# Optimization experiments

Hardware: AMD Instinct MI355X
Metric: run time of the kernel (lower is better)

## Reference

```python
import jax, jax.numpy as jnp
import numpy as np

EPS = 1e-08


def setup_inputs() -> dict:
    key = jax.random.key(0)
    kx, ky = jax.random.split(key)
    x = jax.random.normal(kx, (8192, 512), dtype=jnp.float32)
    y = jax.random.normal(ky, (8192, 512), dtype=jnp.float32)
    return {"x": x, "y": y}


def reference(x, y):
    # Faithful to torch.nn.CosineSimilarity(dim=2, eps=EPS) applied to the
    # broadcast pair (x[i], y[j]):
    #   cos[i, j] = <x_i, y_j> / (max(||x_i||, eps) * max(||y_j||, eps))
    # Algebraically equivalent efficient form: normalize rows once, then GEMM.
    xn = x / jnp.maximum(jnp.linalg.norm(x, axis=1, keepdims=True), EPS)  # [Nx, L]
    yn = y / jnp.maximum(jnp.linalg.norm(y, axis=1, keepdims=True), EPS)  # [Ny, L]
    return jnp.einsum('il,jl->ij', xn, yn)  # [Nx, Ny]
```

## Files before the change

kernel.cpp:

```cpp
#include <hip/hip_runtime.h>


typedef __attribute__((ext_vector_type(8))) short bf16x8;
typedef __attribute__((ext_vector_type(4))) float f32x4;
typedef __attribute__((ext_vector_type(8))) unsigned short ushort8;

#define M_DIM 8192
#define N_DIM 8192
#define K_DIM 512

static __device__ __forceinline__ unsigned short f32_to_bf16(float f) {
  unsigned int u = __float_as_uint(f);
  u = (u + 0x7FFFu + ((u >> 16) & 1u)) >> 16;
  return (unsigned short)u;
}

__global__ __launch_bounds__(256) void normalize_rows(
    const float* __restrict__ x, const float* __restrict__ y,
    unsigned short* __restrict__ out) {
  const int wid = threadIdx.x >> 6;
  const int lane = threadIdx.x & 63;
  const int row = (blockIdx.x << 2) + wid;
  const float* src = row < M_DIM ? x + (size_t)row * K_DIM
                                 : y + (size_t)(row - M_DIM) * K_DIM;
  const float4* r = (const float4*)src;
  float4 v0 = r[lane * 2];
  float4 v1 = r[lane * 2 + 1];
  float ss = v0.x * v0.x + v0.y * v0.y + v0.z * v0.z + v0.w * v0.w +
             v1.x * v1.x + v1.y * v1.y + v1.z * v1.z + v1.w * v1.w;
#pragma unroll
  for (int off = 32; off; off >>= 1) ss += __shfl_xor(ss, off, 64);
  const float s = 1.0f / fmaxf(sqrtf(ss), 1e-8f);
  const float f[8] = {v0.x, v0.y, v0.z, v0.w, v1.x, v1.y, v1.z, v1.w};
  union { ushort8 v; unsigned short u[8]; } o;
#pragma unroll
  for (int i = 0; i < 8; ++i) o.u[i] = f32_to_bf16(f[i] * s);
  *(ushort8*)(out + (size_t)row * K_DIM + lane * 8) = o.v;
}

static __device__ __forceinline__ void gl16(const unsigned short* g, char* l) {
  __builtin_amdgcn_global_load_lds(
      (const __attribute__((address_space(1))) unsigned int*)g,
      (__attribute__((address_space(3))) unsigned int*)l, 16, 0, 0);
}

#define BAR() __builtin_amdgcn_s_barrier()
#define SBAR() __builtin_amdgcn_sched_barrier(0)
#define LGKM0() do { asm volatile("s_waitcnt lgkmcnt(0)" ::: "memory"); \
                     __builtin_amdgcn_sched_barrier(0); } while (0)
#define VMCNT(n) do { asm volatile("s_waitcnt vmcnt(" #n ")" ::: "memory"); \
                      __builtin_amdgcn_sched_barrier(0); } while (0)

__global__ __launch_bounds__(256, 2) void cosgemm(
    const unsigned short* __restrict__ A,
    const unsigned short* __restrict__ B,
    float* __restrict__ C) {
  extern __shared__ char smem[];

  const int tid = threadIdx.x;
  const int lane = tid & 63;
  const int wid = tid >> 6;
  const int wm = wid >> 1;
  const int wn = wid & 1;
  const int lr16 = lane & 15;
  const int hq = lane >> 4;
  const int sw = hq ^ (lr16 & 3);

  const int bid = blockIdx.x;
  const int idx = bid >> 3;
  const int by = ((bid & 7) << 2) + (idx & 3);
  const int bx = idx >> 2;
  const int row0 = by << 8;
  const int col0 = bx << 7;

  const int srl = lane >> 2;
  const int ssl = (lane & 3) ^ (srl & 3);
  const unsigned short* pA =
      A + (size_t)(row0 + (wid << 6) + srl) * K_DIM + ssl * 8;
  const unsigned short* pB =
      B + (size_t)(col0 + (wid << 5) + srl) * K_DIM + ssl * 8;

  auto stageA2 = [&](int par, int cpair, int T) {
    char* l = smem + par * 24576 + (wid << 12) + (cpair << 11);
    const unsigned short* g = pA + T * 32 + (size_t)(cpair << 5) * K_DIM;
    gl16(g, l);
    gl16(g + (size_t)16 * K_DIM, l + 1024);
  };
  auto stageB1 = [&](int par, int c, int T) {
    char* l = smem + par * 24576 + 16384 + (wid << 11) + (c << 10);
    gl16(pB + T * 32 + (size_t)(c << 4) * K_DIM, l);
  };

  bf16x8 af[4], bf[4];
  f32x4 acc[8][4] = {};

  auto ldA = [&](int par, int fmBase) {
#pragma unroll
    for (int j = 0; j < 4; ++j) {
      const int row = (wm << 7) + (fmBase + j) * 16 + lr16;
      af[j] = *(const bf16x8*)(smem + par * 24576 + row * 64 + (sw << 4));
    }
  };
  auto ldB = [&](int par, int fnBase) {
#pragma unroll
    for (int j = 0; j < 2; ++j) {
      const int row = (wn << 6) + (fnBase + j) * 16 + lr16;
      bf[fnBase + j] =
          *(const bf16x8*)(smem + par * 24576 + 16384 + row * 64 + (sw << 4));
    }
  };
  auto mm = [&](int fmBase, int fnBase) {
    __builtin_amdgcn_s_setprio(1);
#pragma unroll
    for (int m = 0; m < 4; ++m)
#pragma unroll
      for (int n = 0; n < 2; ++n)
        acc[fmBase + m][fnBase + n] = __builtin_amdgcn_mfma_f32_16x16x32_bf16(
            af[m], bf[fnBase + n], acc[fmBase + m][fnBase + n], 0, 0, 0);
    __builtin_amdgcn_s_setprio(0);
  };

  stageA2(0, 0, 0); stageA2(0, 1, 0);
  stageB1(0, 0, 0); stageB1(0, 1, 0);
  stageB1(1, 0, 1); stageB1(1, 1, 1);
  VMCNT(2);
  BAR(); SBAR();

#pragma unroll 1
  for (int j = 0; j < 8; ++j) {
    const bool st = (j < 7);
    const int u = 2 * j + 1, t2 = 2 * j + 2, t3 = 2 * j + 3;
    ldA(0, 0); ldB(0, 0); stageA2(1, 0, u);
    BAR(); LGKM0(); mm(0, 0); BAR();
    ldB(0, 2); stageA2(1, 1, u);
    BAR(); LGKM0(); mm(0, 2); BAR();
    ldA(0, 4); if (st) stageB1(0, 0, t2);
    BAR(); LGKM0(); mm(4, 0); BAR();
    if (st) stageB1(0, 1, t2);
    BAR(); LGKM0(); mm(4, 2);
    if (st) { VMCNT(2); } else { VMCNT(0); }
    BAR(); SBAR();
    ldA(1, 0); ldB(1, 0); if (st) stageA2(0, 0, t2);
    BAR(); LGKM0(); mm(0, 0); BAR();
    ldB(1, 2); if (st) stageA2(0, 1, t2);
    BAR(); LGKM0(); mm(0, 2); BAR();
    ldA(1, 4); if (st) stageB1(1, 0, t3);
    BAR(); LGKM0(); mm(4, 0); BAR();
    if (st) stageB1(1, 1, t3);
    BAR(); LGKM0(); mm(4, 2);
    if (st) { VMCNT(2); }
    BAR(); SBAR();
  }

  float* S = (float*)(smem + wid * 4352);
  const int crow0 = row0 + (wm << 7);
  const int ccol0 = col0 + (wn << 6);
#pragma unroll
  for (int fm = 0; fm < 8; ++fm) {
#pragma unroll
    for (int fn = 0; fn < 4; ++fn)
#pragma unroll
      for (int q = 0; q < 4; ++q)
        S[(hq * 4 + q) * 68 + fn * 16 + lr16] = acc[fm][fn][q];
#pragma unroll
    for (int r = 0; r < 4; ++r) {
      f32x4 v = *(const f32x4*)&S[(r * 4 + hq) * 68 + lr16 * 4];
      __builtin_nontemporal_store(
          v, (f32x4*)&C[(size_t)(crow0 + fm * 16 + r * 4 + hq) * N_DIM +
                        ccol0 + lr16 * 4]);
    }
  }
}

extern "C" void kernel_launch(void* const* d_in, const int* in_sizes, int n_in,
                              void* d_out, int out_size, void* d_ws, size_t ws_size,
                              hipStream_t stream) {
  const float* x = (const float*)d_in[0];
  const float* y = (const float*)d_in[1];
  float* out = (float*)d_out;
  unsigned short* xn = (unsigned short*)d_ws;
  unsigned short* yn = xn + (size_t)M_DIM * K_DIM;

  (void)hipFuncSetAttribute((const void*)cosgemm,
                            hipFuncAttributeMaxDynamicSharedMemorySize, 65536);

  normalize_rows<<<(M_DIM + N_DIM) / 4, 256, 0, stream>>>(x, y, xn);
  cosgemm<<<(M_DIM / 256) * (N_DIM / 128), 256, 49152, stream>>>(xn, yn, out);
}
```

Before: 109.5 us.

## Transpose GEMM block tile to 128x256 with 4x1 warp layout and wide-row epilogue

Changes the block tile from 256x128 to 128x256 and rearranges the warps from a 2x2 grid to four warps stacked along M, each computing 32 rows by the full 256 columns. The A/B staging roles and the block-index swizzle are swapped to match. The epilogue now stages 8-row slabs through LDS so each row write covers a contiguous 1 KB stretch, aimed at the large fp32 output write, and it uses plain stores instead of nontemporal ones. The cost is more LDS fragment reads per warp per k-step (B fragments are no longer shared across a warp pair) and more accumulator registers per warp.

```diff
diff --git a/kernel.cpp b/kernel.cpp
--- a/kernel.cpp
+++ b/kernel.cpp
@@ -60,69 +60,67 @@
   const int tid = threadIdx.x;
   const int lane = tid & 63;
   const int wid = tid >> 6;
-  const int wm = wid >> 1;
-  const int wn = wid & 1;
   const int lr16 = lane & 15;
   const int hq = lane >> 4;
   const int sw = hq ^ (lr16 & 3);
 
   const int bid = blockIdx.x;
   const int idx = bid >> 3;
-  const int by = ((bid & 7) << 2) + (idx & 3);
-  const int bx = idx >> 2;
-  const int row0 = by << 8;
-  const int col0 = bx << 7;
+  const int by = ((bid & 7) << 3) + (idx & 7);
+  const int bx = idx >> 3;
+  const int row0 = by << 7;
+  const int col0 = bx << 8;
 
   const int srl = lane >> 2;
   const int ssl = (lane & 3) ^ (srl & 3);
   const unsigned short* pA =
-      A + (size_t)(row0 + (wid << 6) + srl) * K_DIM + ssl * 8;
+      A + (size_t)(row0 + (wid << 5) + srl) * K_DIM + ssl * 8;
   const unsigned short* pB =
-      B + (size_t)(col0 + (wid << 5) + srl) * K_DIM + ssl * 8;
+      B + (size_t)(col0 + (wid << 6) + srl) * K_DIM + ssl * 8;
 
-  auto stageA2 = [&](int par, int cpair, int T) {
-    char* l = smem + par * 24576 + (wid << 12) + (cpair << 11);
-    const unsigned short* g = pA + T * 32 + (size_t)(cpair << 5) * K_DIM;
+  auto stageA1 = [&](int par, int c, int T) {
+    char* l = smem + par * 24576 + (wid << 11) + (c << 10);
+    gl16(pA + T * 32 + (size_t)(c << 4) * K_DIM, l);
+  };
+  auto stageB2 = [&](int par, int cp, int T) {
+    char* l = smem + par * 24576 + 8192 + (wid << 12) + (cp << 11);
+    const unsigned short* g = pB + T * 32 + (size_t)(cp << 5) * K_DIM;
     gl16(g, l);
     gl16(g + (size_t)16 * K_DIM, l + 1024);
   };
-  auto stageB1 = [&](int par, int c, int T) {
-    char* l = smem + par * 24576 + 16384 + (wid << 11) + (c << 10);
-    gl16(pB + T * 32 + (size_t)(c << 4) * K_DIM, l);
+
+  bf16x8 af[2], bf[4];
+  f32x4 acc[2][16] = {};
+
+  auto ldA = [&](int par) {
+#pragma unroll
+    for (int m = 0; m < 2; ++m) {
+      const int row = (wid << 5) + m * 16 + lr16;
+      af[m] = *(const bf16x8*)(smem + par * 24576 + row * 64 + (sw << 4));
+    }
   };
-
-  bf16x8 af[4], bf[4];
-  f32x4 acc[8][4] = {};
-
-  auto ldA = [&](int par, int fmBase) {
+  auto ldB = [&](int par, int g) {
 #pragma unroll
     for (int j = 0; j < 4; ++j) {
-      const int row = (wm << 7) + (fmBase + j) * 16 + lr16;
-      af[j] = *(const bf16x8*)(smem + par * 24576 + row * 64 + (sw << 4));
+      const int row = (g * 4 + j) * 16 + lr16;
+      bf[j] = *(const bf16x8*)(smem + par * 24576 + 8192 + row * 64 +
+                               (sw << 4));
     }
   };
-  auto ldB = [&](int par, int fnBase) {
-#pragma unroll
-    for (int j = 0; j < 2; ++j) {
-      const int row = (wn << 6) + (fnBase + j) * 16 + lr16;
-      bf[fnBase + j] =
-          *(const bf16x8*)(smem + par * 24576 + 16384 + row * 64 + (sw << 4));
-    }
-  };
-  auto mm = [&](int fmBase, int fnBase) {
+  auto mm = [&](int g) {
     __builtin_amdgcn_s_setprio(1);
 #pragma unroll
-    for (int m = 0; m < 4; ++m)
+    for (int m = 0; m < 2; ++m)
 #pragma unroll
-      for (int n = 0; n < 2; ++n)
-        acc[fmBase + m][fnBase + n] = __builtin_amdgcn_mfma_f32_16x16x32_bf16(
-            af[m], bf[fnBase + n], acc[fmBase + m][fnBase + n], 0, 0, 0);
+      for (int j = 0; j < 4; ++j)
+        acc[m][g * 4 + j] = __builtin_amdgcn_mfma_f32_16x16x32_bf16(
+            af[m], bf[j], acc[m][g * 4 + j], 0, 0, 0);
     __builtin_amdgcn_s_setprio(0);
   };
 
-  stageA2(0, 0, 0); stageA2(0, 1, 0);
-  stageB1(0, 0, 0); stageB1(0, 1, 0);
-  stageB1(1, 0, 1); stageB1(1, 1, 1);
+  stageB2(0, 0, 0); stageB2(0, 1, 0);
+  stageA1(0, 0, 0); stageA1(0, 1, 0);
+  stageA1(1, 0, 1); stageA1(1, 1, 1);
   VMCNT(2);
   BAR(); SBAR();
 
@@ -130,46 +128,49 @@
   for (int j = 0; j < 8; ++j) {
     const bool st = (j < 7);
     const int u = 2 * j + 1, t2 = 2 * j + 2, t3 = 2 * j + 3;
-    ldA(0, 0); ldB(0, 0); stageA2(1, 0, u);
-    BAR(); LGKM0(); mm(0, 0); BAR();
-    ldB(0, 2); stageA2(1, 1, u);
-    BAR(); LGKM0(); mm(0, 2); BAR();
-    ldA(0, 4); if (st) stageB1(0, 0, t2);
-    BAR(); LGKM0(); mm(4, 0); BAR();
-    if (st) stageB1(0, 1, t2);
-    BAR(); LGKM0(); mm(4, 2);
+    ldA(0); ldB(0, 0); stageB2(1, 0, u);
+    BAR(); LGKM0(); mm(0); BAR();
+    ldB(0, 1); stageB2(1, 1, u);
+    BAR(); LGKM0(); mm(1); BAR();
+    ldB(0, 2); if (st) stageA1(0, 0, t2);
+    BAR(); LGKM0(); mm(2); BAR();
+    ldB(0, 3); if (st) stageA1(0, 1, t2);
+    BAR(); LGKM0(); mm(3);
     if (st) { VMCNT(2); } else { VMCNT(0); }
     BAR(); SBAR();
-    ldA(1, 0); ldB(1, 0); if (st) stageA2(0, 0, t2);
-    BAR(); LGKM0(); mm(0, 0); BAR();
-    ldB(1, 2); if (st) stageA2(0, 1, t2);
-    BAR(); LGKM0(); mm(0, 2); BAR();
-    ldA(1, 4); if (st) stageB1(1, 0, t3);
-    BAR(); LGKM0(); mm(4, 0); BAR();
-    if (st) stageB1(1, 1, t3);
-    BAR(); LGKM0(); mm(4, 2);
+    ldA(1); ldB(1, 0); if (st) stageB2(0, 0, t2);
+    BAR(); LGKM0(); mm(0); BAR();
+    ldB(1, 1); if (st) stageB2(0, 1, t2);
+    BAR(); LGKM0(); mm(1); BAR();
+    ldB(1, 2); if (st) stageA1(1, 0, t3);
+    BAR(); LGKM0(); mm(2); BAR();
+    ldB(1, 3); if (st) stageA1(1, 1, t3);
+    BAR(); LGKM0(); mm(3);
     if (st) { VMCNT(2); }
     BAR(); SBAR();
   }
 
-  float* S = (float*)(smem + wid * 4352);
-  const int crow0 = row0 + (wm << 7);
-  const int ccol0 = col0 + (wn << 6);
+  float* S = (float*)(smem + wid * 8256);
+  const int crow0 = row0 + (wid << 5);
+  const size_t cbase = (size_t)col0 + lane * 4;
 #pragma unroll
-  for (int fm = 0; fm < 8; ++fm) {
+  for (int fm = 0; fm < 2; ++fm)
 #pragma unroll
-    for (int fn = 0; fn < 4; ++fn)
+    for (int h = 0; h < 2; ++h) {
+      if ((hq >> 1) == h) {
 #pragma unroll
-      for (int q = 0; q < 4; ++q)
-        S[(hq * 4 + q) * 68 + fn * 16 + lr16] = acc[fm][fn][q];
+        for (int fn = 0; fn < 16; ++fn)
 #pragma unroll
-    for (int r = 0; r < 4; ++r) {
-      f32x4 v = *(const f32x4*)&S[(r * 4 + hq) * 68 + lr16 * 4];
-      __builtin_nontemporal_store(
-          v, (f32x4*)&C[(size_t)(crow0 + fm * 16 + r * 4 + hq) * N_DIM +
-                        ccol0 + lr16 * 4]);
+          for (int q = 0; q < 4; ++q)
+            S[((hq & 1) * 4 + q) * 258 + fn * 16 + lr16] = acc[fm][fn][q];
+      }
+      LGKM0();
+#pragma unroll
+      for (int r = 0; r < 8; ++r) {
+        f32x4 v = *(const f32x4*)&S[r * 258 + lane * 4];
+        *(f32x4*)&C[(size_t)(crow0 + fm * 16 + h * 8 + r) * N_DIM + cbase] = v;
+      }
     }
-  }
 }
 
 extern "C" void kernel_launch(void* const* d_in, const int* in_sizes, int n_in,
@@ -185,5 +186,5 @@
                             hipFuncAttributeMaxDynamicSharedMemorySize, 65536);
 
   normalize_rows<<<(M_DIM + N_DIM) / 4, 256, 0, stream>>>(x, y, xn);
-  cosgemm<<<(M_DIM / 256) * (N_DIM / 128), 256, 49152, stream>>>(xn, yn, out);
+  cosgemm<<<(M_DIM / 128) * (N_DIM / 256), 256, 49152, stream>>>(xn, yn, out);
 }
```

Result: slower. 113.5 us (+3.6%).

## Shrink GEMM tile to 128x128 with triple-buffered LDS pipeline and higher occupancy

Applied to the files above, without the earlier changes.

The block tile drops from 256x128 to 128x128, halving the accumulators per wave so that three blocks can fit per CU (launch bounds raised to 3). The double-buffered ping-pong loop becomes a triple-buffered ring with prefetch distance two, and the block-index swizzle is adjusted for the doubled grid. Smaller tiles and more blocks aim to improve latency hiding and load balance across CUs, at the cost of lower arithmetic intensity per tile and more redundant global and L2 traffic.

```diff
diff --git a/kernel.cpp b/kernel.cpp
--- a/kernel.cpp
+++ b/kernel.cpp
@@ -51,7 +51,7 @@
 #define VMCNT(n) do { asm volatile("s_waitcnt vmcnt(" #n ")" ::: "memory"); \
                       __builtin_amdgcn_sched_barrier(0); } while (0)
 
-__global__ __launch_bounds__(256, 2) void cosgemm(
+__global__ __launch_bounds__(256, 3) void cosgemm(
     const unsigned short* __restrict__ A,
     const unsigned short* __restrict__ B,
     float* __restrict__ C) {
@@ -68,95 +68,80 @@
 
   const int bid = blockIdx.x;
   const int idx = bid >> 3;
-  const int by = ((bid & 7) << 2) + (idx & 3);
-  const int bx = idx >> 2;
-  const int row0 = by << 8;
+  const int by = ((bid & 7) << 3) + (idx & 7);
+  const int bx = idx >> 3;
+  const int row0 = by << 7;
   const int col0 = bx << 7;
 
   const int srl = lane >> 2;
   const int ssl = (lane & 3) ^ (srl & 3);
   const unsigned short* pA =
-      A + (size_t)(row0 + (wid << 6) + srl) * K_DIM + ssl * 8;
+      A + (size_t)(row0 + (wid << 4) + srl) * K_DIM + ssl * 8;
   const unsigned short* pB =
-      B + (size_t)(col0 + (wid << 5) + srl) * K_DIM + ssl * 8;
+      B + (size_t)(col0 + (wid << 4) + srl) * K_DIM + ssl * 8;
 
-  auto stageA2 = [&](int par, int cpair, int T) {
-    char* l = smem + par * 24576 + (wid << 12) + (cpair << 11);
-    const unsigned short* g = pA + T * 32 + (size_t)(cpair << 5) * K_DIM;
-    gl16(g, l);
-    gl16(g + (size_t)16 * K_DIM, l + 1024);
+  auto stageA = [&](int buf, int h, int T) {
+    char* l = smem + buf * 16384 + (h << 12) + (wid << 10);
+    gl16(pA + T * 32 + (size_t)(h << 6) * K_DIM, l);
   };
-  auto stageB1 = [&](int par, int c, int T) {
-    char* l = smem + par * 24576 + 16384 + (wid << 11) + (c << 10);
-    gl16(pB + T * 32 + (size_t)(c << 4) * K_DIM, l);
+  auto stageB = [&](int buf, int h, int T) {
+    char* l = smem + buf * 16384 + 8192 + (h << 12) + (wid << 10);
+    gl16(pB + T * 32 + (size_t)(h << 6) * K_DIM, l);
   };
 
   bf16x8 af[4], bf[4];
-  f32x4 acc[8][4] = {};
+  f32x4 acc[4][4] = {};
 
-  auto ldA = [&](int par, int fmBase) {
+  auto ldA = [&](int buf) {
 #pragma unroll
-    for (int j = 0; j < 4; ++j) {
-      const int row = (wm << 7) + (fmBase + j) * 16 + lr16;
-      af[j] = *(const bf16x8*)(smem + par * 24576 + row * 64 + (sw << 4));
+    for (int m = 0; m < 4; ++m) {
+      const int row = (wm << 6) + m * 16 + lr16;
+      af[m] = *(const bf16x8*)(smem + buf * 16384 + row * 64 + (sw << 4));
     }
   };
-  auto ldB = [&](int par, int fnBase) {
+  auto ldB = [&](int buf, int g) {
 #pragma unroll
     for (int j = 0; j < 2; ++j) {
-      const int row = (wn << 6) + (fnBase + j) * 16 + lr16;
-      bf[fnBase + j] =
-          *(const bf16x8*)(smem + par * 24576 + 16384 + row * 64 + (sw << 4));
+      const int row = (wn << 6) + (g * 2 + j) * 16 + lr16;
+      bf[g * 2 + j] = *(const bf16x8*)(smem + buf * 16384 + 8192 + row * 64 +
+                                       (sw << 4));
     }
   };
-  auto mm = [&](int fmBase, int fnBase) {
+  auto mm = [&](int g) {
     __builtin_amdgcn_s_setprio(1);
 #pragma unroll
     for (int m = 0; m < 4; ++m)
 #pragma unroll
-      for (int n = 0; n < 2; ++n)
-        acc[fmBase + m][fnBase + n] = __builtin_amdgcn_mfma_f32_16x16x32_bf16(
-            af[m], bf[fnBase + n], acc[fmBase + m][fnBase + n], 0, 0, 0);
+      for (int j = 0; j < 2; ++j)
+        acc[m][g * 2 + j] = __builtin_amdgcn_mfma_f32_16x16x32_bf16(
+            af[m], bf[g * 2 + j], acc[m][g * 2 + j], 0, 0, 0);
     __builtin_amdgcn_s_setprio(0);
   };
 
-  stageA2(0, 0, 0); stageA2(0, 1, 0);
-  stageB1(0, 0, 0); stageB1(0, 1, 0);
-  stageB1(1, 0, 1); stageB1(1, 1, 1);
-  VMCNT(2);
+  stageA(0, 0, 0); stageA(0, 1, 0); stageB(0, 0, 0); stageB(0, 1, 0);
+  stageA(1, 0, 1); stageA(1, 1, 1); stageB(1, 0, 1); stageB(1, 1, 1);
+  VMCNT(4);
   BAR(); SBAR();
 
 #pragma unroll 1
-  for (int j = 0; j < 8; ++j) {
-    const bool st = (j < 7);
-    const int u = 2 * j + 1, t2 = 2 * j + 2, t3 = 2 * j + 3;
-    ldA(0, 0); ldB(0, 0); stageA2(1, 0, u);
-    BAR(); LGKM0(); mm(0, 0); BAR();
-    ldB(0, 2); stageA2(1, 1, u);
-    BAR(); LGKM0(); mm(0, 2); BAR();
-    ldA(0, 4); if (st) stageB1(0, 0, t2);
-    BAR(); LGKM0(); mm(4, 0); BAR();
-    if (st) stageB1(0, 1, t2);
-    BAR(); LGKM0(); mm(4, 2);
-    if (st) { VMCNT(2); } else { VMCNT(0); }
-    BAR(); SBAR();
-    ldA(1, 0); ldB(1, 0); if (st) stageA2(0, 0, t2);
-    BAR(); LGKM0(); mm(0, 0); BAR();
-    ldB(1, 2); if (st) stageA2(0, 1, t2);
-    BAR(); LGKM0(); mm(0, 2); BAR();
-    ldA(1, 4); if (st) stageB1(1, 0, t3);
-    BAR(); LGKM0(); mm(4, 0); BAR();
-    if (st) stageB1(1, 1, t3);
-    BAR(); LGKM0(); mm(4, 2);
-    if (st) { VMCNT(2); }
+  for (int t = 0; t < 16; ++t) {
+    const int cb = t % 3, nb = (t + 2) % 3;
+    const bool st = (t < 14);
+    ldA(cb); ldB(cb, 0);
+    if (st) { stageA(nb, 0, t + 2); stageA(nb, 1, t + 2); }
+    BAR(); LGKM0(); mm(0); BAR();
+    ldB(cb, 1);
+    if (st) { stageB(nb, 0, t + 2); stageB(nb, 1, t + 2); }
+    BAR(); LGKM0(); mm(1);
+    if (st) { VMCNT(4); } else { VMCNT(0); }
     BAR(); SBAR();
   }
 
   float* S = (float*)(smem + wid * 4352);
-  const int crow0 = row0 + (wm << 7);
+  const int crow0 = row0 + (wm << 6);
   const int ccol0 = col0 + (wn << 6);
 #pragma unroll
-  for (int fm = 0; fm < 8; ++fm) {
+  for (int fm = 0; fm < 4; ++fm) {
 #pragma unroll
     for (int fn = 0; fn < 4; ++fn)
 #pragma unroll
@@ -182,8 +167,8 @@
   unsigned short* yn = xn + (size_t)M_DIM * K_DIM;
 
   (void)hipFuncSetAttribute((const void*)cosgemm,
-                            hipFuncAttributeMaxDynamicSharedMemorySize, 65536);
+                            hipFuncAttributeMaxDynamicSharedMemorySize, 49152);
 
   normalize_rows<<<(M_DIM + N_DIM) / 4, 256, 0, stream>>>(x, y, xn);
-  cosgemm<<<(M_DIM / 256) * (N_DIM / 128), 256, 49152, stream>>>(xn, yn, out);
+  cosgemm<<<(M_DIM / 128) * (N_DIM / 128), 256, 49152, stream>>>(xn, yn, out);
 }
```

Result: no change. 111.1 us (+1.5%).
